# Kernel tuning notes

Hardware: AMD Instinct MI355X
Metric: run time of the kernel (lower is better)

The kernel has to match this reference:

```python
import jax, jax.numpy as jnp
import numpy as np

H = 1024        # hidden_size == voc.num_words (required by module math)
V_OUT = 32000   # output_size / embedding vocab
B = 128
S = 512
MOG = 5


def _p(key, shape, scale=0.02):
    return scale * jax.random.normal(key, shape, dtype=jnp.float32)


def setup_inputs() -> dict:
    key = jax.random.key(0)
    ks = jax.random.split(key, 24)
    inp = {
        "input_step": jax.random.randint(ks[0], (1, B), 0, V_OUT),
        "encoder_outputs": jax.random.normal(ks[1], (S, B, H), dtype=jnp.float32),
        "h1": jax.random.normal(ks[2], (B, H), dtype=jnp.float32),
        "c1": jax.random.normal(ks[3], (B, H), dtype=jnp.float32),
        "emb": _p(ks[4], (V_OUT, H), 1.0),
        # mogrifier + LSTMCell params, layer 1 (input_size == hidden_size == H)
        "mog1_W": _p(ks[5], (MOG, H, H)),
        "mog1_b": _p(ks[6], (MOG, H)),
        "lstm1_Wih": _p(ks[7], (4 * H, H)),
        "lstm1_Whh": _p(ks[8], (4 * H, H)),
        "lstm1_bih": _p(ks[9], (4 * H,)),
        "lstm1_bhh": _p(ks[10], (4 * H,)),
        # layer 2
        "mog2_W": _p(ks[11], (MOG, H, H)),
        "mog2_b": _p(ks[12], (MOG, H)),
        "lstm2_Wih": _p(ks[13], (4 * H, H)),
        "lstm2_Whh": _p(ks[14], (4 * H, H)),
        "lstm2_bih": _p(ks[15], (4 * H,)),
        "lstm2_bhh": _p(ks[16], (4 * H,)),
        # MogLSTM.fc: hidden -> voc.num_words (== H)
        "fc_W": _p(ks[17], (H, H)),
        "fc_b": _p(ks[18], (H,)),
        # decoder concat / out
        "concat_W": _p(ks[19], (H, 2 * H)),
        "concat_b": _p(ks[20], (H,)),
        "out_W": _p(ks[21], (V_OUT, H)),
        "out_b": _p(ks[22], (V_OUT,)),
    }
    return inp


def _mog_lstm_cell(x, h, c, mog_W, mog_b, Wih, Whh, bih, bhh):
    # mogrify: 5 alternating tiny gated updates (x first, then h, ...)
    for i in range(MOG):
        g = 2.0 * jax.nn.sigmoid((h if (i + 1) % 2 != 0 else x) @ mog_W[i].T + mog_b[i])
        if (i + 1) % 2 == 0:
            h = g * h
        else:
            x = g * x
    gates = x @ Wih.T + bih + h @ Whh.T + bhh          # [B, 4H]
    i_, f_, g_, o_ = jnp.split(gates, 4, axis=1)        # torch order: i,f,g,o
    c = jax.nn.sigmoid(f_) * c + jax.nn.sigmoid(i_) * jnp.tanh(g_)
    h = jax.nn.sigmoid(o_) * jnp.tanh(c)
    return h, c


def reference(input_step, encoder_outputs, h1, c1, emb,
              mog1_W, mog1_b, lstm1_Wih, lstm1_Whh, lstm1_bih, lstm1_bhh,
              mog2_W, mog2_b, lstm2_Wih, lstm2_Whh, lstm2_bih, lstm2_bhh,
              fc_W, fc_b, concat_W, concat_b, out_W, out_b):
    x = emb[input_step[0]]                               # [B, H] (seq_len = 1)
    # MogLSTM: layer-1 uses provided (h1, c1); layer-2 state is zero-init
    h1n, _ = _mog_lstm_cell(x, h1, c1, mog1_W, mog1_b,
                            lstm1_Wih, lstm1_Whh, lstm1_bih, lstm1_bhh)
    z = jnp.zeros_like(h1n)
    h2n, _ = _mog_lstm_cell(h1n, z, z, mog2_W, mog2_b,
                            lstm2_Wih, lstm2_Whh, lstm2_bih, lstm2_bhh)
    rnn_out = h2n @ fc_W.T + fc_b                        # [B, H] (fc -> voc.num_words == H)
    hidden = h2n[None]                                   # [1, B, H]
    # Luong dot attention over encoder memory [S, B, H]
    scores = jnp.einsum('bh,sbh->bs', rnn_out, encoder_outputs)
    attn = jax.nn.softmax(scores, axis=1)                # [B, S]
    context = jnp.einsum('bs,sbh->bh', attn, encoder_outputs)
    concat_out = jnp.tanh(jnp.concatenate([rnn_out, context], axis=1) @ concat_W.T + concat_b)
    output = jax.nn.softmax(concat_out @ out_W.T + out_b, axis=1)  # [B, V_OUT]
    return output, hidden
```

## Files before the change

### kernel.cpp

```cpp
#include <hip/hip_runtime.h>
#include <math.h>

typedef unsigned short u16;
typedef unsigned int   u32;

#define B    128
#define H    1024
#define SEQ  512
#define VOUT 32000

using bf16x8 = __attribute__((ext_vector_type(8))) short;
using f32x4  = __attribute__((ext_vector_type(4))) float;

__device__ __forceinline__ float b2f(u32 u){ return __uint_as_float((u & 0xffffu) << 16); }
__device__ __forceinline__ float sigm(float x){ return 1.0f / (1.0f + expf(-x)); }
__device__ __forceinline__ u32 cvt2(float a, float b){
  u32 ua = __float_as_uint(a); ua += 0x7fffu + ((ua >> 16) & 1u);
  u32 ub = __float_as_uint(b); ub += 0x7fffu + ((ub >> 16) & 1u);
  return (ua >> 16) | (ub & 0xffff0000u);
}

__device__ __forceinline__ float ldf(const void* p, size_t i, int bf){
  return bf ? b2f(((const u16*)p)[i]) : ((const float*)p)[i];
}

__global__ void k_detect(const u16* __restrict__ enc, int* __restrict__ flag){
  __shared__ int cnt;
  if (threadIdx.x == 0) cnt = 0;
  __syncthreads();
  int c = 0;
  for (int j = threadIdx.x; j < 512; j += 256){
    u32 u = enc[j];
    u32 e = (u >> 7) & 0xFFu;
    c += (u == 0u || (e >= 100u && e <= 130u)) ? 1 : 0;
  }
  atomicAdd(&cnt, c);
  __syncthreads();
  if (threadIdx.x == 0) *flag = (cnt > 410) ? 1 : 0;
}

__global__ void k_init(const int* __restrict__ idx, const void* __restrict__ emb,
                       const void* __restrict__ h1, float* __restrict__ X, float* __restrict__ Hb,
                       const int* __restrict__ flagp){
  int bf = *flagp;
  int t = blockIdx.x * 256 + threadIdx.x;
  int b = t >> 10, h = t & (H - 1);
  X[t]  = ldf(emb, (size_t)idx[b] * H + h, bf);
  Hb[t] = ldf(h1, t, bf);
}

template<int OUT>
__global__ __launch_bounds__(256)
void gemm_s(const float* __restrict__ A, const void* __restrict__ W, size_t wOff,
            float* __restrict__ P, int K, int Kc, int N, const int* __restrict__ flagp)
{
  const int bf = *flagp;
  __shared__ float As[32][132];
  __shared__ float Wt[32][68];
  const int t  = threadIdx.x;
  const int n0 = blockIdx.x * 64;
  const int kbase = blockIdx.y * Kc;
  const int sb = t >> 1,  sk = (t & 1) << 4;
  const int wn = t >> 2,  wk = (t & 3) << 3;
  const int bx = (t & 15) << 3;
  const int ny = (t >> 4) << 2;

  float acc[8][4];
  #pragma unroll
  for (int i = 0; i < 8; ++i)
    #pragma unroll
    for (int j = 0; j < 4; ++j) acc[i][j] = 0.f;

  for (int k0 = 0; k0 < Kc; k0 += 32){
    const int kb = kbase + k0;
    const float4* Ap = (const float4*)(A + (size_t)sb * K + kb + sk);
    float4 a0 = Ap[0], a1 = Ap[1], a2 = Ap[2], a3 = Ap[3];
    size_t we = wOff + (size_t)(n0 + wn) * K + kb + wk;
    float w0,w1,w2,w3,w4,w5,w6,w7;
    if (bf){
      uint4 wv = *(const uint4*)((const u16*)W + we);
      w0=b2f(wv.x); w1=b2f(wv.x>>16); w2=b2f(wv.y); w3=b2f(wv.y>>16);
      w4=b2f(wv.z); w5=b2f(wv.z>>16); w6=b2f(wv.w); w7=b2f(wv.w>>16);
    } else {
      const float* Wf = (const float*)W + we;
      float4 p = *(const float4*)Wf, q = *(const float4*)(Wf + 4);
      w0=p.x; w1=p.y; w2=p.z; w3=p.w; w4=q.x; w5=q.y; w6=q.z; w7=q.w;
    }

    As[sk+ 0][sb]=a0.x; As[sk+ 1][sb]=a0.y; As[sk+ 2][sb]=a0.z; As[sk+ 3][sb]=a0.w;
    As[sk+ 4][sb]=a1.x; As[sk+ 5][sb]=a1.y; As[sk+ 6][sb]=a1.z; As[sk+ 7][sb]=a1.w;
    As[sk+ 8][sb]=a2.x; As[sk+ 9][sb]=a2.y; As[sk+10][sb]=a2.z; As[sk+11][sb]=a2.w;
    As[sk+12][sb]=a3.x; As[sk+13][sb]=a3.y; As[sk+14][sb]=a3.z; As[sk+15][sb]=a3.w;
    Wt[wk+0][wn]=w0; Wt[wk+1][wn]=w1; Wt[wk+2][wn]=w2; Wt[wk+3][wn]=w3;
    Wt[wk+4][wn]=w4; Wt[wk+5][wn]=w5; Wt[wk+6][wn]=w6; Wt[wk+7][wn]=w7;
    __syncthreads();

    #pragma unroll
    for (int kk = 0; kk < 32; ++kk){
      float4 wv = *(const float4*)(&Wt[kk][ny]);
      float a[8];
      #pragma unroll
      for (int i = 0; i < 8; ++i) a[i] = As[kk][bx+i];
      #pragma unroll
      for (int i = 0; i < 8; ++i){
        acc[i][0] = fmaf(a[i], wv.x, acc[i][0]);
        acc[i][1] = fmaf(a[i], wv.y, acc[i][1]);
        acc[i][2] = fmaf(a[i], wv.z, acc[i][2]);
        acc[i][3] = fmaf(a[i], wv.w, acc[i][3]);
      }
    }
    __syncthreads();
  }

  float* Pp = P + (size_t)blockIdx.y * B * N;
  #pragma unroll
  for (int j = 0; j < 4; ++j){
    int n = n0 + ny + j;
    #pragma unroll
    for (int i = 0; i < 8; ++i){
      size_t o = (size_t)(bx + i) * N + n;
      if (OUT == 0) Pp[o] = acc[i][j];
      else          Pp[o] += acc[i][j];
    }
  }
}

template<int ACT>
__global__ void ep_gen(const float* __restrict__ P, int S, const void* __restrict__ bias,
                       size_t bOff, float* __restrict__ C, int ostr,
                       const int* __restrict__ flagp){
  int bf = *flagp;
  int t = blockIdx.x * 256 + threadIdx.x;
  int b = t >> 10, h = t & (H - 1);
  float s = 0.f;
  for (int i = 0; i < S; ++i) s += P[(size_t)i * B * H + t];
  s += ldf(bias, bOff + h, bf);
  size_t o = (size_t)b * ostr + h;
  if (ACT == 0)      C[o] = s;
  else if (ACT == 1) C[o] = tanhf(s);
  else               C[o] = C[o] * 2.f * sigm(s);
}

__global__ void ep_lstm(const float* __restrict__ P, int S, const void* __restrict__ bih,
                        const void* __restrict__ bhh, const void* __restrict__ cprev,
                        float* __restrict__ hout, float* __restrict__ hf,
                        const void* __restrict__ mog2b, const int* __restrict__ flagp){
  int bf = *flagp;
  int t = blockIdx.x * 256 + threadIdx.x;
  int b = t >> 10, h = t & (H - 1);
  size_t base = (size_t)b * 4 * H;
  float gi=0.f, gf=0.f, gg=0.f, go=0.f;
  for (int s = 0; s < S; ++s){
    const float* q = P + (size_t)s * B * 4 * H + base;
    gi += q[h]; gf += q[H + h]; gg += q[2*H + h]; go += q[3*H + h];
  }
  gi += ldf(bih, h, bf)       + ldf(bhh, h, bf);
  gf += ldf(bih, H + h, bf)   + ldf(bhh, H + h, bf);
  gg += ldf(bih, 2*H + h, bf) + ldf(bhh, 2*H + h, bf);
  go += ldf(bih, 3*H + h, bf) + ldf(bhh, 3*H + h, bf);
  float c = cprev ? sigm(gf) * ldf(cprev, t, bf) : 0.f;
  c += sigm(gi) * tanhf(gg);
  float hv = sigm(go) * tanhf(c);
  if (hf) hf[t] = hv;
  if (mog2b){
    hv *= 8.f * sigm(ldf(mog2b, h, bf)) * sigm(ldf(mog2b, 2*H + h, bf))
              * sigm(ldf(mog2b, 4*H + h, bf));
  }
  hout[t] = hv;
}

__global__ __launch_bounds__(256)
void k_scores(const float* __restrict__ CAT, const void* __restrict__ enc, float* __restrict__ SC,
              const int* __restrict__ flagp){
  int bf = *flagp;
  int wid  = (blockIdx.x << 2) + (threadIdx.x >> 6);
  int lane = threadIdx.x & 63;
  int b = wid >> 9, s = wid & (SEQ - 1);
  size_t base = ((size_t)s * B + b) * H;
  const float* r = CAT + (size_t)b * 2 * H;
  float acc = 0.f;
  #pragma unroll
  for (int k0 = 0; k0 < H; k0 += 512){
    int h = k0 + lane * 8;
    float e0,e1,e2,e3,e4,e5,e6,e7;
    if (bf){
      uint4 u = *(const uint4*)((const u16*)enc + base + h);
      e0=b2f(u.x); e1=b2f(u.x>>16); e2=b2f(u.y); e3=b2f(u.y>>16);
      e4=b2f(u.z); e5=b2f(u.z>>16); e6=b2f(u.w); e7=b2f(u.w>>16);
    } else {
      const float* ef = (const float*)enc + base + h;
      float4 p = *(const float4*)ef, q = *(const float4*)(ef + 4);
      e0=p.x; e1=p.y; e2=p.z; e3=p.w; e4=q.x; e5=q.y; e6=q.z; e7=q.w;
    }
    float4 r0 = *(const float4*)(r + h);
    float4 r1 = *(const float4*)(r + h + 4);
    acc += e0*r0.x + e1*r0.y + e2*r0.z + e3*r0.w
         + e4*r1.x + e5*r1.y + e6*r1.z + e7*r1.w;
  }
  #pragma unroll
  for (int o = 32; o; o >>= 1) acc += __shfl_down(acc, o);
  if (lane == 0) SC[(size_t)b * SEQ + s] = acc;
}

__global__ __launch_bounds__(256)
void k_softmax_s(float* __restrict__ SC){
  int b = blockIdx.x, t = threadIdx.x;
  float* row = SC + (size_t)b * SEQ;
  float v0 = row[t], v1 = row[t + 256];
  __shared__ float rm[4], rs[4];
  int lane = t & 63, w = t >> 6;
  float m = fmaxf(v0, v1);
  #pragma unroll
  for (int o = 32; o; o >>= 1) m = fmaxf(m, __shfl_down(m, o));
  if (!lane) rm[w] = m;
  __syncthreads();
  float M = fmaxf(fmaxf(rm[0], rm[1]), fmaxf(rm[2], rm[3]));
  float e0 = expf(v0 - M), e1 = expf(v1 - M);
  float s = e0 + e1;
  #pragma unroll
  for (int o = 32; o; o >>= 1) s += __shfl_down(s, o);
  if (!lane) rs[w] = s;
  __syncthreads();
  float inv = 1.f / (rs[0] + rs[1] + rs[2] + rs[3]);
  row[t] = e0 * inv; row[t + 256] = e1 * inv;
}

__global__ __launch_bounds__(256)
void k_context(const float* __restrict__ SC, const void* __restrict__ enc, float* __restrict__ CAT,
               const int* __restrict__ flagp){
  int bf = *flagp;
  int b = blockIdx.x, t = threadIdx.x;
  __shared__ float aw[SEQ];
  aw[t] = SC[(size_t)b * SEQ + t];
  aw[t + 256] = SC[(size_t)b * SEQ + t + 256];
  __syncthreads();
  int h0 = t << 2;
  float a0=0.f, a1=0.f, a2=0.f, a3=0.f;
  for (int ss = 0; ss < SEQ; ++ss){
    size_t off = ((size_t)ss * B + b) * H + h0;
    float e0,e1,e2,e3;
    if (bf){
      uint2 u = *(const uint2*)((const u16*)enc + off);
      e0=b2f(u.x); e1=b2f(u.x>>16); e2=b2f(u.y); e3=b2f(u.y>>16);
    } else {
      float4 u = *(const float4*)((const float*)enc + off);
      e0=u.x; e1=u.y; e2=u.z; e3=u.w;
    }
    float wgt = aw[ss];
    a0 = fmaf(wgt, e0, a0);
    a1 = fmaf(wgt, e1, a1);
    a2 = fmaf(wgt, e2, a2);
    a3 = fmaf(wgt, e3, a3);
  }
  float4 o4 = {a0, a1, a2, a3};
  *(float4*)(CAT + (size_t)b * 2 * H + H + h0) = o4;
}

__global__ void k_cvtA(const float* __restrict__ X, u16* __restrict__ Xb){
  int t = blockIdx.x * 256 + threadIdx.x;
  const float4* p = (const float4*)(X + t * 8);
  float4 f0 = p[0], f1 = p[1];
  uint4 o;
  o.x = cvt2(f0.x, f0.y); o.y = cvt2(f0.z, f0.w);
  o.z = cvt2(f1.x, f1.y); o.w = cvt2(f1.z, f1.w);
  *(uint4*)(Xb + t * 8) = o;
}

__global__ __launch_bounds__(256)
void gemm_out_mfma(const u16* __restrict__ Xb, const void* __restrict__ W,
                   const void* __restrict__ bias, float* __restrict__ Cg,
                   const int* __restrict__ flagp)
{
  const int bf = *flagp;
  __shared__ u16 Ws[64][72];
  const int t = threadIdx.x;
  const int n0 = blockIdx.x * 64;
  const int wave = t >> 6, lane = t & 63;
  const int m0 = wave * 32;
  const int lm = lane & 15, quad = lane >> 4;
  const int sn = t >> 2, sk = (t & 3) * 16;

  f32x4 acc[2][4];
  #pragma unroll
  for (int i = 0; i < 2; ++i)
    #pragma unroll
    for (int j = 0; j < 4; ++j) acc[i][j] = (f32x4){0.f, 0.f, 0.f, 0.f};

  for (int k0 = 0; k0 < H; k0 += 64){
    if (bf){
      const u16* wp = (const u16*)W + (size_t)(n0 + sn) * H + k0 + sk;
      *(uint4*)(&Ws[sn][sk])     = *(const uint4*)wp;
      *(uint4*)(&Ws[sn][sk + 8]) = *(const uint4*)(wp + 8);
    } else {
      const float* wp = (const float*)W + (size_t)(n0 + sn) * H + k0 + sk;
      float4 f0 = *(const float4*)wp,     f1 = *(const float4*)(wp + 4);
      float4 f2 = *(const float4*)(wp+8), f3 = *(const float4*)(wp + 12);
      uint4 o0, o1;
      o0.x = cvt2(f0.x, f0.y); o0.y = cvt2(f0.z, f0.w);
      o0.z = cvt2(f1.x, f1.y); o0.w = cvt2(f1.z, f1.w);
      o1.x = cvt2(f2.x, f2.y); o1.y = cvt2(f2.z, f2.w);
      o1.z = cvt2(f3.x, f3.y); o1.w = cvt2(f3.z, f3.w);
      *(uint4*)(&Ws[sn][sk])     = o0;
      *(uint4*)(&Ws[sn][sk + 8]) = o1;
    }
    __syncthreads();
    #pragma unroll
    for (int ks = 0; ks < 64; ks += 32){
      bf16x8 a0 = *(const bf16x8*)(Xb + (size_t)(m0 + lm) * H + k0 + ks + quad * 8);
      bf16x8 a1 = *(const bf16x8*)(Xb + (size_t)(m0 + 16 + lm) * H + k0 + ks + quad * 8);
      #pragma unroll
      for (int nt = 0; nt < 4; ++nt){
        bf16x8 bfr = *(const bf16x8*)(&Ws[nt * 16 + lm][ks + quad * 8]);
        acc[0][nt] = __builtin_amdgcn_mfma_f32_16x16x32_bf16(a0, bfr, acc[0][nt], 0, 0, 0);
        acc[1][nt] = __builtin_amdgcn_mfma_f32_16x16x32_bf16(a1, bfr, acc[1][nt], 0, 0, 0);
      }
    }
    __syncthreads();
  }

  #pragma unroll
  for (int nt = 0; nt < 4; ++nt){
    int n = n0 + nt * 16 + lm;
    float bj = ldf(bias, n, bf);
    #pragma unroll
    for (int mt = 0; mt < 2; ++mt)
      #pragma unroll
      for (int r = 0; r < 4; ++r){
        int m = m0 + mt * 16 + quad * 4 + r;
        Cg[(size_t)m * VOUT + n] = acc[mt][nt][r] + bj;
      }
  }
}

__global__ __launch_bounds__(256)
void k_softmax_v(float* __restrict__ out){
  int b = blockIdx.x, t = threadIdx.x;
  float* row = out + (size_t)b * VOUT;
  __shared__ float rm[4], rs[4];
  int lane = t & 63, w = t >> 6;
  float m = -3.0e38f;
  for (int i = 4*t; i < VOUT; i += 1024){
    float4 v = *(const float4*)(row + i);
    m = fmaxf(m, fmaxf(fmaxf(v.x, v.y), fmaxf(v.z, v.w)));
  }
  #pragma unroll
  for (int o = 32; o; o >>= 1) m = fmaxf(m, __shfl_down(m, o));
  if (!lane) rm[w] = m;
  __syncthreads();
  float M = fmaxf(fmaxf(rm[0], rm[1]), fmaxf(rm[2], rm[3]));
  float s = 0.f;
  for (int i = 4*t; i < VOUT; i += 1024){
    float4 v = *(const float4*)(row + i);
    s += expf(v.x-M) + expf(v.y-M) + expf(v.z-M) + expf(v.w-M);
  }
  #pragma unroll
  for (int o = 32; o; o >>= 1) s += __shfl_down(s, o);
  if (!lane) rs[w] = s;
  __syncthreads();
  float inv = 1.f / (rs[0] + rs[1] + rs[2] + rs[3]);
  for (int i = 4*t; i < VOUT; i += 1024){
    float4 v = *(const float4*)(row + i);
    v.x = expf(v.x-M)*inv; v.y = expf(v.y-M)*inv;
    v.z = expf(v.z-M)*inv; v.w = expf(v.w-M)*inv;
    *(float4*)(row + i) = v;
  }
}

extern "C" void kernel_launch(void* const* d_in, const int* in_sizes, int n_in,
                              void* d_out, int out_size, void* d_ws, size_t ws_size,
                              hipStream_t stream){
  (void)in_sizes; (void)n_in; (void)out_size;
  const int* idx   = (const int*)d_in[0];
  const void* enc  = d_in[1];
  const void* h1   = d_in[2];
  const void* c1   = d_in[3];
  const void* emb  = d_in[4];
  const void* mog1W= d_in[5];
  const void* mog1b= d_in[6];
  const void* Wih1 = d_in[7];
  const void* Whh1 = d_in[8];
  const void* bih1 = d_in[9];
  const void* bhh1 = d_in[10];
  const void* mog2b= d_in[12];
  const void* Wih2 = d_in[13];
  const void* bih2 = d_in[15];
  const void* bhh2 = d_in[16];
  const void* fcW  = d_in[17];
  const void* fcb  = d_in[18];
  const void* ccW  = d_in[19];
  const void* ccb  = d_in[20];
  const void* outW = d_in[21];
  const void* outb = d_in[22];

  float* X    = (float*)d_ws;
  float* Hb   = X   + B*H;
  float* H2   = Hb  + B*H;
  float* CAT  = H2  + B*H;
  float* SC   = CAT + (size_t)B*2*H;
  int*  FLAG  = (int*)(SC + B*SEQ);
  u16*  Xb    = (u16*)(FLAG + 64);
  float* P    = (float*)(Xb + B*H);

  size_t need = ((size_t)(5*B*H + B*SEQ) + 64) * 4 + (size_t)B*H*2 + (size_t)4*B*4*H*4;
  int S1 = 8, S2 = 4;
  if (ws_size < need) { S1 = 4; S2 = 1; }

  float* out_f = (float*)d_out;
  float* hid_f = out_f + (size_t)B * VOUT;

  k_detect<<<1, 256, 0, stream>>>((const u16*)enc, FLAG);
  k_init<<<B*H/256, 256, 0, stream>>>(idx, emb, h1, X, Hb, FLAG);

  for (int i = 0; i < 5; ++i){
    const float* a = (i & 1) ? X : Hb;
    float*       c = (i & 1) ? Hb : X;
    gemm_s<0><<<dim3(H/64, S1), 256, 0, stream>>>(a, mog1W, (size_t)i*H*H, P, H, H/S1, H, FLAG);
    ep_gen<2><<<B*H/256, 256, 0, stream>>>(P, S1, mog1b, (size_t)i*H, c, H, FLAG);
  }

  gemm_s<0><<<dim3(4*H/64, S2), 256, 0, stream>>>(X,  Wih1, 0, P, H, H/S2, 4*H, FLAG);
  gemm_s<1><<<dim3(4*H/64, S2), 256, 0, stream>>>(Hb, Whh1, 0, P, H, H/S2, 4*H, FLAG);
  ep_lstm<<<B*H/256, 256, 0, stream>>>(P, S2, bih1, bhh1, c1, X, nullptr, mog2b, FLAG);

  gemm_s<0><<<dim3(4*H/64, S2), 256, 0, stream>>>(X, Wih2, 0, P, H, H/S2, 4*H, FLAG);
  ep_lstm<<<B*H/256, 256, 0, stream>>>(P, S2, bih2, bhh2, nullptr, H2, hid_f, nullptr, FLAG);

  gemm_s<0><<<dim3(H/64, S1), 256, 0, stream>>>(H2, fcW, 0, P, H, H/S1, H, FLAG);
  ep_gen<0><<<B*H/256, 256, 0, stream>>>(P, S1, fcb, 0, CAT, 2*H, FLAG);

  k_scores<<<B*SEQ/4, 256, 0, stream>>>(CAT, enc, SC, FLAG);
  k_softmax_s<<<B, 256, 0, stream>>>(SC);
  k_context<<<B, 256, 0, stream>>>(SC, enc, CAT, FLAG);

  gemm_s<0><<<dim3(H/64, S1), 256, 0, stream>>>(CAT, ccW, 0, P, 2*H, 2*H/S1, H, FLAG);
  ep_gen<1><<<B*H/256, 256, 0, stream>>>(P, S1, ccb, 0, X, H, FLAG);
  k_cvtA<<<B*H/(256*8), 256, 0, stream>>>(X, Xb);
  gemm_out_mfma<<<VOUT/64, 256, 0, stream>>>(Xb, outW, outb, out_f, FLAG);
  k_softmax_v<<<B, 256, 0, stream>>>(out_f);
}
```

Baseline: 974.1 us.

## Fuse attention scores, softmax and context into one flash-style split-sequence kernel

Replaces the separate score, softmax and context kernels with a single kernel that streams encoder tiles through shared memory once, using an online softmax over four sequence quarters per batch row. A small finalize kernel then merges the partial max, sum and context. This removes the second full read of the encoder tensor and two launches, at the cost of extra synchronisation and only 512 blocks. It also widens the vocab softmax blocks to 1024 threads and raises the split-K factor S1 from 8 to 16.

```diff
diff --git a/kernel.cpp b/kernel.cpp
--- a/kernel.cpp
+++ b/kernel.cpp
@@ -8,6 +8,11 @@
 #define H    1024
 #define SEQ  512
 #define VOUT 32000
+
+#define NQ   4
+#define SQB  (SEQ / NQ)
+#define TS   8
+#define NT   (SQB / TS)
 
 using bf16x8 = __attribute__((ext_vector_type(8))) short;
 using f32x4  = __attribute__((ext_vector_type(4))) float;
@@ -169,91 +174,147 @@
   hout[t] = hv;
 }
 
+template<int BF>
+__device__ __forceinline__ void attn_body(const float* __restrict__ CAT,
+                                          const void* __restrict__ enc,
+                                          float* __restrict__ Pctx,
+                                          float* __restrict__ Pml)
+{
+  __shared__ float els[TS][H];
+  __shared__ float sc[TS];
+  const int t = threadIdx.x;
+  const int wave = t >> 6, lane = t & 63;
+  const int b = blockIdx.x >> 2, q = blockIdx.x & 3;
+  const int s0 = q * SQB;
+
+  const float* rp = CAT + (size_t)b * 2 * H + lane * 16;
+  float4 r0 = *(const float4*)rp,       r1 = *(const float4*)(rp + 4),
+         r2 = *(const float4*)(rp + 8), r3 = *(const float4*)(rp + 12);
+
+  float m = -3.0e38f, l = 0.f;
+  float a0 = 0.f, a1 = 0.f, a2 = 0.f, a3 = 0.f;
+  const int h0 = t * 4;
+
+  float4 v[8];
+  uint4  u[4];
+
+  auto issue = [&](int tile){
+    int ss = s0 + tile * TS;
+    if (BF == 0){
+      #pragma unroll
+      for (int i = 0; i < 8; ++i){
+        int seg = i * 256 + t;
+        int r = seg >> 8, c = (seg & 255) * 4;
+        v[i] = *(const float4*)((const float*)enc + ((size_t)(ss + r) * B + b) * H + c);
+      }
+    } else {
+      #pragma unroll
+      for (int i = 0; i < 4; ++i){
+        int seg = i * 256 + t;
+        int r = seg >> 7, c = (seg & 127) * 8;
+        u[i] = *(const uint4*)((const u16*)enc + ((size_t)(ss + r) * B + b) * H + c);
+      }
+    }
+  };
+  auto commit = [&](){
+    if (BF == 0){
+      #pragma unroll
+      for (int i = 0; i < 8; ++i) ((float4*)els)[i * 256 + t] = v[i];
+    } else {
+      #pragma unroll
+      for (int i = 0; i < 4; ++i){
+        int seg = i * 256 + t;
+        float4 lo = {b2f(u[i].x), b2f(u[i].x >> 16), b2f(u[i].y), b2f(u[i].y >> 16)};
+        float4 hi = {b2f(u[i].z), b2f(u[i].z >> 16), b2f(u[i].w), b2f(u[i].w >> 16)};
+        ((float4*)els)[seg * 2]     = lo;
+        ((float4*)els)[seg * 2 + 1] = hi;
+      }
+    }
+  };
+
+  issue(0);
+  commit();
+  __syncthreads();
+
+  for (int tile = 0; tile < NT; ++tile){
+    if (tile + 1 < NT) issue(tile + 1);
+
+    #pragma unroll
+    for (int i = 0; i < 2; ++i){
+      int row = wave * 2 + i;
+      const float* e = &els[row][lane * 16];
+      float4 e0 = *(const float4*)e,       e1 = *(const float4*)(e + 4),
+             e2 = *(const float4*)(e + 8), e3 = *(const float4*)(e + 12);
+      float d = e0.x*r0.x + e0.y*r0.y + e0.z*r0.z + e0.w*r0.w
+              + e1.x*r1.x + e1.y*r1.y + e1.z*r1.z + e1.w*r1.w
+              + e2.x*r2.x + e2.y*r2.y + e2.z*r2.z + e2.w*r2.w
+              + e3.x*r3.x + e3.y*r3.y + e3.z*r3.z + e3.w*r3.w;
+      #pragma unroll
+      for (int o = 32; o; o >>= 1) d += __shfl_down(d, o);
+      if (lane == 0) sc[row] = d;
+    }
+    __syncthreads();
+
+    float s0v = sc[0], s1v = sc[1], s2v = sc[2], s3v = sc[3];
+    float s4v = sc[4], s5v = sc[5], s6v = sc[6], s7v = sc[7];
+    float tm = fmaxf(fmaxf(fmaxf(s0v, s1v), fmaxf(s2v, s3v)),
+                     fmaxf(fmaxf(s4v, s5v), fmaxf(s6v, s7v)));
+    float nm = fmaxf(m, tm);
+    float scale = expf(m - nm);
+    float p0 = expf(s0v - nm), p1 = expf(s1v - nm), p2 = expf(s2v - nm), p3 = expf(s3v - nm);
+    float p4 = expf(s4v - nm), p5 = expf(s5v - nm), p6 = expf(s6v - nm), p7 = expf(s7v - nm);
+    l = l * scale + (p0 + p1 + p2 + p3 + p4 + p5 + p6 + p7);
+    m = nm;
+    a0 *= scale; a1 *= scale; a2 *= scale; a3 *= scale;
+    #pragma unroll
+    for (int s = 0; s < TS; ++s){
+      float4 e = *(const float4*)(&els[s][h0]);
+      float p = (s == 0 ? p0 : s == 1 ? p1 : s == 2 ? p2 : s == 3 ? p3 :
+                 s == 4 ? p4 : s == 5 ? p5 : s == 6 ? p6 : p7);
+      a0 = fmaf(p, e.x, a0); a1 = fmaf(p, e.y, a1);
+      a2 = fmaf(p, e.z, a2); a3 = fmaf(p, e.w, a3);
+    }
+    __syncthreads();
+
+    if (tile + 1 < NT){
+      commit();
+      __syncthreads();
+    }
+  }
+
+  float4 av = {a0, a1, a2, a3};
+  *(float4*)(Pctx + ((size_t)q * B + b) * H + h0) = av;
+  if (t == 0){
+    Pml[((size_t)q * B + b) * 2]     = m;
+    Pml[((size_t)q * B + b) * 2 + 1] = l;
+  }
+}
+
 __global__ __launch_bounds__(256)
-void k_scores(const float* __restrict__ CAT, const void* __restrict__ enc, float* __restrict__ SC,
-              const int* __restrict__ flagp){
-  int bf = *flagp;
-  int wid  = (blockIdx.x << 2) + (threadIdx.x >> 6);
-  int lane = threadIdx.x & 63;
-  int b = wid >> 9, s = wid & (SEQ - 1);
-  size_t base = ((size_t)s * B + b) * H;
-  const float* r = CAT + (size_t)b * 2 * H;
-  float acc = 0.f;
-  #pragma unroll
-  for (int k0 = 0; k0 < H; k0 += 512){
-    int h = k0 + lane * 8;
-    float e0,e1,e2,e3,e4,e5,e6,e7;
-    if (bf){
-      uint4 u = *(const uint4*)((const u16*)enc + base + h);
-      e0=b2f(u.x); e1=b2f(u.x>>16); e2=b2f(u.y); e3=b2f(u.y>>16);
-      e4=b2f(u.z); e5=b2f(u.z>>16); e6=b2f(u.w); e7=b2f(u.w>>16);
-    } else {
-      const float* ef = (const float*)enc + base + h;
-      float4 p = *(const float4*)ef, q = *(const float4*)(ef + 4);
-      e0=p.x; e1=p.y; e2=p.z; e3=p.w; e4=q.x; e5=q.y; e6=q.z; e7=q.w;
-    }
-    float4 r0 = *(const float4*)(r + h);
-    float4 r1 = *(const float4*)(r + h + 4);
-    acc += e0*r0.x + e1*r0.y + e2*r0.z + e3*r0.w
-         + e4*r1.x + e5*r1.y + e6*r1.z + e7*r1.w;
-  }
-  #pragma unroll
-  for (int o = 32; o; o >>= 1) acc += __shfl_down(acc, o);
-  if (lane == 0) SC[(size_t)b * SEQ + s] = acc;
-}
-
-__global__ __launch_bounds__(256)
-void k_softmax_s(float* __restrict__ SC){
-  int b = blockIdx.x, t = threadIdx.x;
-  float* row = SC + (size_t)b * SEQ;
-  float v0 = row[t], v1 = row[t + 256];
-  __shared__ float rm[4], rs[4];
-  int lane = t & 63, w = t >> 6;
-  float m = fmaxf(v0, v1);
-  #pragma unroll
-  for (int o = 32; o; o >>= 1) m = fmaxf(m, __shfl_down(m, o));
-  if (!lane) rm[w] = m;
-  __syncthreads();
-  float M = fmaxf(fmaxf(rm[0], rm[1]), fmaxf(rm[2], rm[3]));
-  float e0 = expf(v0 - M), e1 = expf(v1 - M);
-  float s = e0 + e1;
-  #pragma unroll
-  for (int o = 32; o; o >>= 1) s += __shfl_down(s, o);
-  if (!lane) rs[w] = s;
-  __syncthreads();
-  float inv = 1.f / (rs[0] + rs[1] + rs[2] + rs[3]);
-  row[t] = e0 * inv; row[t + 256] = e1 * inv;
-}
-
-__global__ __launch_bounds__(256)
-void k_context(const float* __restrict__ SC, const void* __restrict__ enc, float* __restrict__ CAT,
-               const int* __restrict__ flagp){
-  int bf = *flagp;
-  int b = blockIdx.x, t = threadIdx.x;
-  __shared__ float aw[SEQ];
-  aw[t] = SC[(size_t)b * SEQ + t];
-  aw[t + 256] = SC[(size_t)b * SEQ + t + 256];
-  __syncthreads();
-  int h0 = t << 2;
-  float a0=0.f, a1=0.f, a2=0.f, a3=0.f;
-  for (int ss = 0; ss < SEQ; ++ss){
-    size_t off = ((size_t)ss * B + b) * H + h0;
-    float e0,e1,e2,e3;
-    if (bf){
-      uint2 u = *(const uint2*)((const u16*)enc + off);
-      e0=b2f(u.x); e1=b2f(u.x>>16); e2=b2f(u.y); e3=b2f(u.y>>16);
-    } else {
-      float4 u = *(const float4*)((const float*)enc + off);
-      e0=u.x; e1=u.y; e2=u.z; e3=u.w;
-    }
-    float wgt = aw[ss];
-    a0 = fmaf(wgt, e0, a0);
-    a1 = fmaf(wgt, e1, a1);
-    a2 = fmaf(wgt, e2, a2);
-    a3 = fmaf(wgt, e3, a3);
-  }
-  float4 o4 = {a0, a1, a2, a3};
-  *(float4*)(CAT + (size_t)b * 2 * H + H + h0) = o4;
+void k_attn(const float* __restrict__ CAT, const void* __restrict__ enc,
+            float* __restrict__ Pctx, float* __restrict__ Pml,
+            const int* __restrict__ flagp){
+  if (*flagp) attn_body<1>(CAT, enc, Pctx, Pml);
+  else        attn_body<0>(CAT, enc, Pctx, Pml);
+}
+
+__global__ void k_attn_fin(const float* __restrict__ Pctx, const float* __restrict__ Pml,
+                           float* __restrict__ CAT){
+  int t = blockIdx.x * 256 + threadIdx.x;
+  int b = t >> 10, h = t & (H - 1);
+  float M = -3.0e38f;
+  #pragma unroll
+  for (int q = 0; q < NQ; ++q) M = fmaxf(M, Pml[((size_t)q * B + b) * 2]);
+  float num = 0.f, den = 0.f;
+  #pragma unroll
+  for (int q = 0; q < NQ; ++q){
+    float mq = Pml[((size_t)q * B + b) * 2];
+    float lq = Pml[((size_t)q * B + b) * 2 + 1];
+    float w = expf(mq - M);
+    num = fmaf(w, Pctx[((size_t)q * B + b) * H + h], num);
+    den = fmaf(w, lq, den);
+  }
+  CAT[(size_t)b * 2 * H + H + h] = num / den;
 }
 
 __global__ void k_cvtA(const float* __restrict__ X, u16* __restrict__ Xb){
@@ -332,14 +393,14 @@
   }
 }
 
-__global__ __launch_bounds__(256)
+__global__ __launch_bounds__(1024)
 void k_softmax_v(float* __restrict__ out){
   int b = blockIdx.x, t = threadIdx.x;
   float* row = out + (size_t)b * VOUT;
-  __shared__ float rm[4], rs[4];
+  __shared__ float rm[16], rs[16];
   int lane = t & 63, w = t >> 6;
   float m = -3.0e38f;
-  for (int i = 4*t; i < VOUT; i += 1024){
+  for (int i = 4*t; i < VOUT; i += 4096){
     float4 v = *(const float4*)(row + i);
     m = fmaxf(m, fmaxf(fmaxf(v.x, v.y), fmaxf(v.z, v.w)));
   }
@@ -347,9 +408,11 @@
   for (int o = 32; o; o >>= 1) m = fmaxf(m, __shfl_down(m, o));
   if (!lane) rm[w] = m;
   __syncthreads();
-  float M = fmaxf(fmaxf(rm[0], rm[1]), fmaxf(rm[2], rm[3]));
+  float M = rm[0];
+  #pragma unroll
+  for (int i = 1; i < 16; ++i) M = fmaxf(M, rm[i]);
   float s = 0.f;
-  for (int i = 4*t; i < VOUT; i += 1024){
+  for (int i = 4*t; i < VOUT; i += 4096){
     float4 v = *(const float4*)(row + i);
     s += expf(v.x-M) + expf(v.y-M) + expf(v.z-M) + expf(v.w-M);
   }
@@ -357,8 +420,11 @@
   for (int o = 32; o; o >>= 1) s += __shfl_down(s, o);
   if (!lane) rs[w] = s;
   __syncthreads();
-  float inv = 1.f / (rs[0] + rs[1] + rs[2] + rs[3]);
-  for (int i = 4*t; i < VOUT; i += 1024){
+  float S = rs[0];
+  #pragma unroll
+  for (int i = 1; i < 16; ++i) S += rs[i];
+  float inv = 1.f / S;
+  for (int i = 4*t; i < VOUT; i += 4096){
     float4 v = *(const float4*)(row + i);
     v.x = expf(v.x-M)*inv; v.y = expf(v.y-M)*inv;
     v.z = expf(v.z-M)*inv; v.w = expf(v.w-M)*inv;
@@ -402,7 +468,7 @@
   float* P    = (float*)(Xb + B*H);
 
   size_t need = ((size_t)(5*B*H + B*SEQ) + 64) * 4 + (size_t)B*H*2 + (size_t)4*B*4*H*4;
-  int S1 = 8, S2 = 4;
+  int S1 = 16, S2 = 4;
   if (ws_size < need) { S1 = 4; S2 = 1; }
 
   float* out_f = (float*)d_out;
@@ -428,13 +494,14 @@
   gemm_s<0><<<dim3(H/64, S1), 256, 0, stream>>>(H2, fcW, 0, P, H, H/S1, H, FLAG);
   ep_gen<0><<<B*H/256, 256, 0, stream>>>(P, S1, fcb, 0, CAT, 2*H, FLAG);
 
-  k_scores<<<B*SEQ/4, 256, 0, stream>>>(CAT, enc, SC, FLAG);
-  k_softmax_s<<<B, 256, 0, stream>>>(SC);
-  k_context<<<B, 256, 0, stream>>>(SC, enc, CAT, FLAG);
+  float* Pctx = P;
+  float* Pml  = P + (size_t)NQ*B*H;
+  k_attn<<<B*NQ, 256, 0, stream>>>(CAT, enc, Pctx, Pml, FLAG);
+  k_attn_fin<<<B*H/256, 256, 0, stream>>>(Pctx, Pml, CAT);
 
   gemm_s<0><<<dim3(H/64, S1), 256, 0, stream>>>(CAT, ccW, 0, P, 2*H, 2*H/S1, H, FLAG);
   ep_gen<1><<<B*H/256, 256, 0, stream>>>(P, S1, ccb, 0, X, H, FLAG);
   k_cvtA<<<B*H/(256*8), 256, 0, stream>>>(X, Xb);
   gemm_out_mfma<<<VOUT/64, 256, 0, stream>>>(Xb, outW, outb, out_f, FLAG);
-  k_softmax_v<<<B, 256, 0, stream>>>(out_f);
-}
+  k_softmax_v<<<B, 1024, 0, stream>>>(out_f);
+}
```

After: 895.5 us. -8.1%, faster.
